# Kernel tuning notes

Measured on AMD Instinct MI355X. Metric: run time of the kernel, lower is better.

## Reference

```python
import jax, jax.numpy as jnp
import numpy as np
from jax import lax

B, T, D, A, H, C, K = 32, 1500, 512, 512, 4, 10, 100  # batch, frames, key/query/value dim, attn dim, heads, conv channels, conv half-kernel


def setup_inputs() -> dict:
    rng = jax.random.key(0)
    ks = jax.random.split(rng, 13)
    s = 0.02  # param init scale
    return {
        "key": jax.random.normal(ks[0], (B, T, D), jnp.float32),
        "key_lens": jax.random.randint(ks[1], (B,), 3 * T // 4, T + 1, jnp.int32),
        "value": jax.random.normal(ks[2], (B, T, D), jnp.float32),
        "query": jax.random.normal(ks[3], (B, 1, D), jnp.float32),
        "aw": jax.random.uniform(ks[4], (H, B, T), jnp.float32),
        # shared-across-heads linear params (ModuleList([m]*n_heads) shares one module)
        "w_enc_W": jax.random.normal(ks[5], (D, A), jnp.float32) * s,
        "w_enc_b": jnp.zeros((A,), jnp.float32),
        "w_dec_W": jax.random.normal(ks[6], (D, A), jnp.float32) * s,
        "w_conv_W": jax.random.normal(ks[7], (C, A), jnp.float32) * s,
        "v_W": jax.random.normal(ks[8], (A,), jnp.float32) * s,
        # distinct conv kernel per head: grouped-conv layout [H*C, 1, 2K+1]
        "conv_W": jax.random.normal(ks[9], (H * C, 1, 2 * K + 1), jnp.float32) * s,
        "w_out_W": jax.random.normal(ks[10], (D * H, D), jnp.float32) * s,
        "w_out_b": jnp.zeros((D,), jnp.float32),
    }


def reference(key, key_lens, value, query, aw, w_enc_W, w_enc_b, w_dec_W,
              w_conv_W, v_W, conv_W, w_out_W, w_out_b):
    bs, key_len, _ = key.shape
    n_heads = aw.shape[0]
    half_k = (conv_W.shape[-1] - 1) // 2

    # key projection (shared weights => identical key_a for every head): [B,T,A]
    key_a = jnp.einsum('btd,da->bta', key, w_enc_W) + w_enc_b
    # query projection (no bias): [B,1,A]
    dec = jnp.einsum('bqd,da->bqa', query, w_dec_W)

    # location conv feature: distinct kernel per head via grouped 1D conv
    x = jnp.transpose(aw, (1, 0, 2))  # [B,H,T]
    conv_out = lax.conv_general_dilated(
        x, conv_W, window_strides=(1,), padding=[(half_k, half_k)],
        feature_group_count=n_heads,
        dimension_numbers=('NCH', 'OIH', 'NCH'))  # [B,H*C,T]
    conv_feat = jnp.transpose(
        conv_out.reshape(bs, n_heads, -1, key_len), (1, 0, 3, 2))  # [H,B,T,C]
    conv_proj = jnp.einsum('hbtc,ca->hbta', conv_feat, w_conv_W)  # [H,B,T,A]

    # additive score with tanh, reduced by v: [H,B,T]
    e = jnp.einsum('hbta,a->hbt',
                   jnp.tanh(key_a[None] + dec[None] + conv_proj), v_W)

    # length mask + softmax (sharpening_factor=1, no sigmoid smoothing)
    mask = jnp.arange(key_len) < key_lens[:, None]  # [B,T]
    e = jnp.where(mask[None], e, -jnp.inf)
    aw_new = jax.nn.softmax(e, axis=-1)  # [H,B,T]

    # NOTE: source uses the INPUT aw for the context (quirk preserved)
    ctx = jnp.einsum('hbt,btv->bhv', aw, value)  # [B,H,V]
    ctx = ctx.reshape(bs, 1, -1)  # head-major concat, [B,1,H*V]
    out = jnp.einsum('bqk,kd->bqd', ctx, w_out_W) + w_out_b  # [B,1,D]
    return out, aw_new
```

## Files before the change

### kernel.cpp

```cpp
#include <hip/hip_runtime.h>
#include <hip/hip_bf16.h>

#define BB 32
#define TT 1500
#define DD 512
#define AA 512
#define HH 4
#define CC 10
#define KK 100
#define KW 201
#define MM (BB*TT)
#define PS 2.8853900817779268f

typedef unsigned short u16;
typedef unsigned int u32;
typedef __attribute__((ext_vector_type(8))) short bf16x8;
typedef __attribute__((ext_vector_type(4))) float f32x4;
typedef __attribute__((ext_vector_type(4))) unsigned int u32x4;

static __device__ __forceinline__ u16 f2bf(float f) {
    u32 x = __float_as_uint(f);
    return (u16)((x + 0x7fffu + ((x >> 16) & 1u)) >> 16);
}
static __device__ __forceinline__ u32 pkbf(float lo, float hi) {
    u32 r;
    asm("v_cvt_pk_bf16_f32 %0, %1, %2" : "=v"(r) : "v"(lo), "v"(hi));
    return r;
}
static __device__ __forceinline__ void stage16(const void* g, void* l) {
    __builtin_amdgcn_global_load_lds(
        (const __attribute__((address_space(1))) void*)g,
        (__attribute__((address_space(3))) void*)l, 16, 0, 0);
}

__global__ __launch_bounds__(256) void prep_k(
    const float* __restrict__ wencW, const float* __restrict__ q,
    const float* __restrict__ wdec, const float* __restrict__ encb,
    const float* __restrict__ aw, const float* __restrict__ convW,
    u16* __restrict__ wenc_t, float* __restrict__ dec_ps,
    float* __restrict__ cfeat, float* __restrict__ ctx, float* __restrict__ outz)
{
    __shared__ float pls[4160];
    int blk = blockIdx.x, tid = threadIdx.x;
    if (blk < 64) {
        int a0 = (blk & 7) * 64, d0 = (blk >> 3) * 64;
#pragma unroll
        for (int it = 0; it < 16; ++it) {
            int row = it * 4 + (tid >> 6), col = tid & 63;
            pls[row * 65 + col] = wencW[(size_t)(d0 + row) * AA + a0 + col];
        }
        __syncthreads();
#pragma unroll
        for (int it = 0; it < 16; ++it) {
            int ar = it * 4 + (tid >> 6), dc = tid & 63;
            wenc_t[(size_t)(a0 + ar) * DD + d0 + dc] = f2bf(pls[dc * 65 + ar] * PS);
        }
    } else if (blk < 128) {
        int bidx = blk - 64;
        int b = bidx >> 1, a = (bidx & 1) * 256 + tid;
        for (int i = tid; i < DD; i += 256) pls[i] = q[b * DD + i];
        __syncthreads();
        float acc = encb[a];
#pragma unroll 8
        for (int d = 0; d < DD; ++d) acc = fmaf(pls[d], wdec[(size_t)d * AA + a], acc);
        dec_ps[b * AA + a] = acc * PS;
    } else if (blk < 384) {
        int cidx = blk - 128;
        int half = cidx & 1, hb = cidx >> 1;
        int h = hb >> 5, b = hb & 31;
        float* srow = pls;
        float* swk  = pls + 952;
        int tstart = half * 750;
        const float* arow = aw + (size_t)(h * BB + b) * TT;
        for (int i = tid; i < 952; i += 256) {
            int t = tstart + i - KK;
            srow[i] = (t >= 0 && t < TT) ? arow[t] : 0.f;
        }
        for (int i = tid; i < CC * KW; i += 256) swk[i] = convW[h * CC * KW + i];
        __syncthreads();
        if (tid < 250) {
            int tl = tid * 3;
            float acc[CC][3];
#pragma unroll
            for (int c = 0; c < CC; ++c)
#pragma unroll
                for (int u = 0; u < 3; ++u) acc[c][u] = 0.f;
            float r0 = srow[tl], r1 = srow[tl + 1], r2 = srow[tl + 2];
            for (int j = 0; j < KW; ++j) {
#pragma unroll
                for (int c = 0; c < CC; ++c) {
                    float w = swk[c * KW + j];
                    acc[c][0] = fmaf(r0, w, acc[c][0]);
                    acc[c][1] = fmaf(r1, w, acc[c][1]);
                    acc[c][2] = fmaf(r2, w, acc[c][2]);
                }
                r0 = r1; r1 = r2; r2 = srow[tl + j + 3];
            }
            float* dst = cfeat + ((size_t)h * MM + (size_t)b * TT + tstart + tl) * CC;
#pragma unroll
            for (int u = 0; u < 3; ++u)
#pragma unroll
                for (int c = 0; c < CC; ++c) dst[u * CC + c] = acc[c][u];
        }
    } else if (blk < 392) {
        float4* p = (float4*)ctx;
        int bidx = blk - 384;
        float4 z = {0.f, 0.f, 0.f, 0.f};
#pragma unroll
        for (int k2 = 0; k2 < 8; ++k2) p[bidx * 2048 + k2 * 256 + tid] = z;
    } else {
        float4* p = (float4*)outz;
        int bidx = blk - 392;
        float4 z = {0.f, 0.f, 0.f, 0.f};
#pragma unroll
        for (int k2 = 0; k2 < 8; ++k2) p[bidx * 2048 + k2 * 256 + tid] = z;
    }
}

__global__ __launch_bounds__(256) void gemm_e_k(
    const float* __restrict__ key, const u16* __restrict__ Bt,
    const float* __restrict__ dec_ps, const float* __restrict__ cf,
    const float* __restrict__ wconv, const float* __restrict__ vw,
    float* __restrict__ Q4)
{
    __shared__ u32x4 smem4[2305];
    char* smem = (char*)smem4;

    int tid = threadIdx.x;
    int orig = blockIdx.x;
    int xcd = orig & 7, idx = orig >> 3;
    int swz = (xcd < 4 ? xcd * 188 : 752 + (xcd - 4) * 187) + idx;
    int bn = swz & 3, bm = swz >> 2;
    int row0 = bm * 128, col0 = bn * 128;
    int lane = tid & 63;
    int wv = tid >> 6;
    int wr = wv >> 1, wc = wv & 1;
    int lhi = lane >> 4, llo = lane & 15;

    f32x4 acc[4][4];
#pragma unroll
    for (int i = 0; i < 4; ++i)
#pragma unroll
        for (int j = 0; j < 4; ++j) acc[i][j] = (f32x4){0.f, 0.f, 0.f, 0.f};

    const float4* gA = (const float4*)(key + (size_t)(row0 + (tid >> 1)) * DD) + (tid & 1) * 4;
    u32 aWoff = (tid >> 1) * 80 + (tid & 1) * 32;
    const u16* gBa = Bt + (size_t)(col0 + (tid & 127)) * DD + (tid >> 7) * 8;
    const u16* gBb = gBa + 16;

    auto loadPA = [&](float4& a0, float4& a1, float4& a2, float4& a3, int s) {
        a0 = gA[s * 8]; a1 = gA[s * 8 + 1]; a2 = gA[s * 8 + 2]; a3 = gA[s * 8 + 3];
    };
    auto stageB = [&](int s, int bbyte) {
        stage16(gBa + s * 32, (u16*)(smem + bbyte) + (size_t)tid * 8);
        stage16(gBb + s * 32, (u16*)(smem + bbyte + 4096) + (size_t)tid * 8);
    };
    auto writeA = [&](int abyte, float4 q0, float4 q1, float4 q2, float4 q3) {
        u32x4 s0, s1;
        s0.x = pkbf(q0.x, q0.y); s0.y = pkbf(q0.z, q0.w);
        s0.z = pkbf(q1.x, q1.y); s0.w = pkbf(q1.z, q1.w);
        s1.x = pkbf(q2.x, q2.y); s1.y = pkbf(q2.z, q2.w);
        s1.z = pkbf(q3.x, q3.y); s1.w = pkbf(q3.z, q3.w);
        *(u32x4*)(smem + abyte + aWoff) = s0;
        *(u32x4*)(smem + abyte + aWoff + 16) = s1;
    };
    auto kstep = [&](int aoff, int boff) {
        bf16x8 af[4], bfr[4];
#pragma unroll
        for (int i = 0; i < 4; ++i)
            af[i] = *(const bf16x8*)(smem + aoff + (wr * 64 + i * 16 + llo) * 80 + lhi * 16);
#pragma unroll
        for (int j = 0; j < 4; ++j)
            bfr[j] = *(const bf16x8*)(smem + boff + (wc * 64 + j * 16 + llo) * 16 + lhi * 2048);
#pragma unroll
        for (int i = 0; i < 4; ++i)
#pragma unroll
            for (int j = 0; j < 4; ++j)
                acc[i][j] = __builtin_amdgcn_mfma_f32_16x16x32_bf16(
                    af[i], bfr[j], acc[i][j], 0, 0, 0);
    };

    float4 e0, e1, e2, e3, o0, o1, o2, o3;
    loadPA(e0, e1, e2, e3, 0);
    stageB(0, 10240);
    writeA(0, e0, e1, e2, e3);
    loadPA(o0, o1, o2, o3, 1);
    loadPA(e0, e1, e2, e3, 2);
    __syncthreads();

#pragma unroll
    for (int t = 0; t < 16; t += 2) {
        stageB(t + 1, 28672);
        writeA(18432, o0, o1, o2, o3);
        if (t + 3 < 16) loadPA(o0, o1, o2, o3, t + 3);
        kstep(0, 10240);
        __syncthreads();
        if (t + 2 < 16) {
            stageB(t + 2, 10240);
            writeA(0, e0, e1, e2, e3);
            if (t + 4 < 16) loadPA(e0, e1, e2, e3, t + 4);
        }
        kstep(18432, 28672);
        __syncthreads();
    }

    const int ZPAD = 36864;
    int b0 = row0 / TT;
    int boundary = (b0 + 1) * TT - row0;
    int b1 = min(b0 + 1, BB - 1);
    {
        int h = tid >> 6;
#pragma unroll
        for (int e = 0; e < 2; ++e) {
            int r = (tid & 63) * 2 + e;
            const float2* cp = (const float2*)(cf + ((size_t)h * MM + row0 + r) * CC);
            float2 c0 = cp[0], c1 = cp[1], c2 = cp[2], c3 = cp[3], c4 = cp[4];
            u32x4 lo, hi;
            lo.x = pkbf(c0.x, c0.y); lo.y = pkbf(c1.x, c1.y);
            lo.z = pkbf(c2.x, c2.y); lo.w = pkbf(c3.x, c3.y);
            hi.x = pkbf(c4.x, c4.y);
            hi.y = (r < boundary) ? 0x00003f80u : 0x3f800000u;
            hi.z = 0u; hi.w = 0u;
            char* dst = smem + (h * 128 + r) * 32;
            *(u32x4*)dst = lo;
            *(u32x4*)(dst + 16) = hi;
        }
        int col = tid >> 1, kh = tid & 1;
        u32x4 w;
        if (kh == 0) {
            float v0 = wconv[0 * AA + col0 + col] * PS, v1 = wconv[1 * AA + col0 + col] * PS;
            float v2 = wconv[2 * AA + col0 + col] * PS, v3 = wconv[3 * AA + col0 + col] * PS;
            float v4 = wconv[4 * AA + col0 + col] * PS, v5 = wconv[5 * AA + col0 + col] * PS;
            float v6 = wconv[6 * AA + col0 + col] * PS, v7 = wconv[7 * AA + col0 + col] * PS;
            w.x = pkbf(v0, v1); w.y = pkbf(v2, v3); w.z = pkbf(v4, v5); w.w = pkbf(v6, v7);
        } else {
            float v8 = wconv[8 * AA + col0 + col] * PS, v9 = wconv[9 * AA + col0 + col] * PS;
            float d0v = dec_ps[b0 * AA + col0 + col], d1v = dec_ps[b1 * AA + col0 + col];
            w.x = pkbf(v8, v9); w.y = pkbf(d0v, d1v); w.z = 0u; w.w = 0u;
        }
        *(u32x4*)(smem + 16384 + col * 32 + kh * 16) = w;
        if (tid == 0) { *(u32x4*)(smem + ZPAD) = (u32x4){0u, 0u, 0u, 0u}; }
    }
    __syncthreads();

    float svj[4];
    bf16x8 be[4];
#pragma unroll
    for (int j = 0; j < 4; ++j) {
        int col = wc * 64 + j * 16 + llo;
        svj[j] = vw[col0 + col];
        u32 off = (lhi < 2) ? (16384u + col * 32 + lhi * 16) : (u32)ZPAD;
        be[j] = *(const bf16x8*)(smem + off);
    }
#pragma unroll
    for (int h = 0; h < 4; ++h) {
#pragma unroll
        for (int i = 0; i < 4; ++i) {
            int rowA = h * 128 + wr * 64 + i * 16 + llo;
            u32 offa = (lhi < 2) ? (rowA * 32 + lhi * 16) : (u32)ZPAD;
            bf16x8 ae = *(const bf16x8*)(smem + offa);
            float ep[4] = {0.f, 0.f, 0.f, 0.f};
#pragma unroll
            for (int j = 0; j < 4; ++j) {
                f32x4 t4 = __builtin_amdgcn_mfma_f32_16x16x32_bf16(ae, be[j], acc[i][j], 0, 0, 0);
#pragma unroll
                for (int r = 0; r < 4; ++r) {
                    float z = exp2f(t4[r]);
                    float p = __builtin_amdgcn_rcpf(1.f + z);
                    ep[r] = fmaf(svj[j], p, ep[r]);
                }
            }
#pragma unroll
            for (int r = 0; r < 4; ++r) {
                float s = ep[r];
                s += __shfl_xor(s, 1);
                s += __shfl_xor(s, 2);
                s += __shfl_xor(s, 4);
                s += __shfl_xor(s, 8);
                if (llo == 0)
                    Q4[((size_t)(bn * HH + h)) * MM + row0 + wr * 64 + i * 16 + lhi * 4 + r] = s;
            }
        }
    }
}

__global__ __launch_bounds__(256) void fin_k(
    const float* __restrict__ Q4, const int* __restrict__ klen,
    const float* __restrict__ aw, const float* __restrict__ value,
    float* __restrict__ aw_new, float* __restrict__ ctx)
{
    __shared__ float fls[1512];
    int blk = blockIdx.x, tid = threadIdx.x;
    if (blk < 128) {
        int h = blk >> 5, b = blk & 31;
        int len = klen[b];
        const float* q0 = Q4 + (size_t)(0 * HH + h) * MM + (size_t)b * TT;
        const float* q1 = Q4 + (size_t)(1 * HH + h) * MM + (size_t)b * TT;
        const float* q2 = Q4 + (size_t)(2 * HH + h) * MM + (size_t)b * TT;
        const float* q3 = Q4 + (size_t)(3 * HH + h) * MM + (size_t)b * TT;
        float* orow = aw_new + (size_t)(h * BB + b) * TT;
        float* rbuf = fls + 1500;
        int lane = tid & 63, wvv = tid >> 6;
        float mx = -3.4e38f;
        for (int t = tid; t < len; t += 256) {
            float e = -2.f * (q0[t] + q1[t] + q2[t] + q3[t]);
            fls[t] = e;
            mx = fmaxf(mx, e);
        }
#pragma unroll
        for (int off = 32; off; off >>= 1) mx = fmaxf(mx, __shfl_xor(mx, off));
        if (lane == 0) rbuf[wvv] = mx;
        __syncthreads();
        mx = fmaxf(fmaxf(rbuf[0], rbuf[1]), fmaxf(rbuf[2], rbuf[3]));
        float sum = 0.f;
        for (int t = tid; t < len; t += 256) {
            float p = __expf(fls[t] - mx);
            fls[t] = p; sum += p;
        }
#pragma unroll
        for (int off = 32; off; off >>= 1) sum += __shfl_xor(sum, off);
        if (lane == 0) rbuf[4 + wvv] = sum;
        __syncthreads();
        float inv = 1.f / (rbuf[4] + rbuf[5] + rbuf[6] + rbuf[7]);
        for (int t = tid; t < TT; t += 256) orow[t] = (t < len) ? fls[t] * inv : 0.f;
    } else {
        int cidx = blk - 128;
        int b = cidx / 25, chunk = cidx - b * 25;
        int c0 = chunk * 60;
        float (*sw)[60] = (float(*)[60])fls;
        if (tid < 240)
            sw[tid / 60][tid % 60] = aw[(size_t)((tid / 60) * BB + b) * TT + c0 + (tid % 60)];
        __syncthreads();
        float a00 = 0, a01 = 0, a10 = 0, a11 = 0, a20 = 0, a21 = 0, a30 = 0, a31 = 0;
        const float* vp = value + ((size_t)b * TT + c0) * DD;
        for (int t = 0; t < 60; ++t) {
            float v0 = vp[(size_t)t * DD + tid];
            float v1 = vp[(size_t)t * DD + tid + 256];
            a00 = fmaf(sw[0][t], v0, a00); a01 = fmaf(sw[0][t], v1, a01);
            a10 = fmaf(sw[1][t], v0, a10); a11 = fmaf(sw[1][t], v1, a11);
            a20 = fmaf(sw[2][t], v0, a20); a21 = fmaf(sw[2][t], v1, a21);
            a30 = fmaf(sw[3][t], v0, a30); a31 = fmaf(sw[3][t], v1, a31);
        }
        atomicAdd(&ctx[(b * HH + 0) * DD + tid], a00);
        atomicAdd(&ctx[(b * HH + 0) * DD + tid + 256], a01);
        atomicAdd(&ctx[(b * HH + 1) * DD + tid], a10);
        atomicAdd(&ctx[(b * HH + 1) * DD + tid + 256], a11);
        atomicAdd(&ctx[(b * HH + 2) * DD + tid], a20);
        atomicAdd(&ctx[(b * HH + 2) * DD + tid + 256], a21);
        atomicAdd(&ctx[(b * HH + 3) * DD + tid], a30);
        atomicAdd(&ctx[(b * HH + 3) * DD + tid + 256], a31);
    }
}

__global__ __launch_bounds__(512) void out_k(const float* __restrict__ ctx,
                                             const float* __restrict__ wout,
                                             const float* __restrict__ wob,
                                             float* __restrict__ out)
{
    int b0 = blockIdx.x * 4, kc = blockIdx.y;
    int tid = threadIdx.x;
    __shared__ float sc[4][64];
    if (tid < 256) sc[tid >> 6][tid & 63] =
        ctx[(size_t)(b0 + (tid >> 6)) * (HH * DD) + kc * 64 + (tid & 63)];
    __syncthreads();
    float acc0 = 0, acc1 = 0, acc2 = 0, acc3 = 0;
    const float* wp = wout + (size_t)(kc * 64) * DD + tid;
#pragma unroll 8
    for (int kk = 0; kk < 64; ++kk) {
        float w = wp[(size_t)kk * DD];
        acc0 = fmaf(sc[0][kk], w, acc0); acc1 = fmaf(sc[1][kk], w, acc1);
        acc2 = fmaf(sc[2][kk], w, acc2); acc3 = fmaf(sc[3][kk], w, acc3);
    }
    if (kc == 0) {
        float bb = wob[tid];
        acc0 += bb; acc1 += bb; acc2 += bb; acc3 += bb;
    }
    atomicAdd(&out[(b0 + 0) * DD + tid], acc0);
    atomicAdd(&out[(b0 + 1) * DD + tid], acc1);
    atomicAdd(&out[(b0 + 2) * DD + tid], acc2);
    atomicAdd(&out[(b0 + 3) * DD + tid], acc3);
}

extern "C" void kernel_launch(void* const* d_in, const int* in_sizes, int n_in,
                              void* d_out, int out_size, void* d_ws, size_t ws_size,
                              hipStream_t stream) {
    const float* key    = (const float*)d_in[0];
    const int*   klen   = (const int*)  d_in[1];
    const float* value  = (const float*)d_in[2];
    const float* query  = (const float*)d_in[3];
    const float* aw     = (const float*)d_in[4];
    const float* wencW  = (const float*)d_in[5];
    const float* wencb  = (const float*)d_in[6];
    const float* wdecW  = (const float*)d_in[7];
    const float* wconvW = (const float*)d_in[8];
    const float* vW     = (const float*)d_in[9];
    const float* convW  = (const float*)d_in[10];
    const float* woutW  = (const float*)d_in[11];
    const float* woutb  = (const float*)d_in[12];

    float* out    = (float*)d_out;
    float* aw_new = out + BB * DD;

    char* ws = (char*)d_ws;
    u16*   wenc_t = (u16*)ws;
    float* dec_ps = (float*)(ws + 524288);
    float* cfeat  = (float*)(ws + 589824);
    float* Q4     = (float*)(ws + 8269824);
    float* ctx    = (float*)(ws + 11341824);

    prep_k  <<<394, 256, 0, stream>>>(wencW, query, wdecW, wencb, aw, convW,
                                      wenc_t, dec_ps, cfeat, ctx, out);
    gemm_e_k<<<1500, 256, 0, stream>>>(key, wenc_t, dec_ps, cfeat, wconvW, vW, Q4);
    fin_k   <<<928, 256, 0, stream>>>(Q4, klen, aw, value, aw_new, ctx);
    out_k   <<<dim3(8, 32), 512, 0, stream>>>(ctx, woutW, woutb, out);
}
```

Baseline: 374.6 us.

## Halve GEMM M-tile to 64 rows and split location conv into more blocks

The fused key-projection/score GEMM now uses 64-row tiles instead of 128, doubling the grid to 3000 blocks. It also shrinks shared memory and moves to a simple double-buffered pipeline with one k-step per iteration. The location-conv stage in the prep kernel is split into 6 chunks per (head,batch) row with one output per thread, increasing block count from 256 to 768. The aim is better occupancy and load balance across the CUs, at the cost of re-reading the B operand more often and less register reuse per thread.

```diff
diff --git a/kernel.cpp b/kernel.cpp
--- a/kernel.cpp
+++ b/kernel.cpp
@@ -64,53 +64,43 @@
 #pragma unroll 8
         for (int d = 0; d < DD; ++d) acc = fmaf(pls[d], wdec[(size_t)d * AA + a], acc);
         dec_ps[b * AA + a] = acc * PS;
-    } else if (blk < 384) {
+    } else if (blk < 896) {
         int cidx = blk - 128;
-        int half = cidx & 1, hb = cidx >> 1;
+        int hb = cidx / 6, chunk = cidx - hb * 6;
         int h = hb >> 5, b = hb & 31;
         float* srow = pls;
-        float* swk  = pls + 952;
-        int tstart = half * 750;
+        float* swk  = pls + 456;
+        int tstart = chunk * 250;
         const float* arow = aw + (size_t)(h * BB + b) * TT;
-        for (int i = tid; i < 952; i += 256) {
+        for (int i = tid; i < 450; i += 256) {
             int t = tstart + i - KK;
             srow[i] = (t >= 0 && t < TT) ? arow[t] : 0.f;
         }
         for (int i = tid; i < CC * KW; i += 256) swk[i] = convW[h * CC * KW + i];
         __syncthreads();
         if (tid < 250) {
-            int tl = tid * 3;
-            float acc[CC][3];
-#pragma unroll
-            for (int c = 0; c < CC; ++c)
-#pragma unroll
-                for (int u = 0; u < 3; ++u) acc[c][u] = 0.f;
-            float r0 = srow[tl], r1 = srow[tl + 1], r2 = srow[tl + 2];
+            float acc[CC];
+#pragma unroll
+            for (int c = 0; c < CC; ++c) acc[c] = 0.f;
             for (int j = 0; j < KW; ++j) {
-#pragma unroll
-                for (int c = 0; c < CC; ++c) {
-                    float w = swk[c * KW + j];
-                    acc[c][0] = fmaf(r0, w, acc[c][0]);
-                    acc[c][1] = fmaf(r1, w, acc[c][1]);
-                    acc[c][2] = fmaf(r2, w, acc[c][2]);
-                }
-                r0 = r1; r1 = r2; r2 = srow[tl + j + 3];
+                float x = srow[tid + j];
+#pragma unroll
+                for (int c = 0; c < CC; ++c)
+                    acc[c] = fmaf(x, swk[c * KW + j], acc[c]);
             }
-            float* dst = cfeat + ((size_t)h * MM + (size_t)b * TT + tstart + tl) * CC;
-#pragma unroll
-            for (int u = 0; u < 3; ++u)
-#pragma unroll
-                for (int c = 0; c < CC; ++c) dst[u * CC + c] = acc[c][u];
-        }
-    } else if (blk < 392) {
+            float* dst = cfeat + ((size_t)h * MM + (size_t)b * TT + tstart + tid) * CC;
+#pragma unroll
+            for (int c = 0; c < CC; ++c) dst[c] = acc[c];
+        }
+    } else if (blk < 904) {
         float4* p = (float4*)ctx;
-        int bidx = blk - 384;
+        int bidx = blk - 896;
         float4 z = {0.f, 0.f, 0.f, 0.f};
 #pragma unroll
         for (int k2 = 0; k2 < 8; ++k2) p[bidx * 2048 + k2 * 256 + tid] = z;
     } else {
         float4* p = (float4*)outz;
-        int bidx = blk - 392;
+        int bidx = blk - 904;
         float4 z = {0.f, 0.f, 0.f, 0.f};
 #pragma unroll
         for (int k2 = 0; k2 < 8; ++k2) p[bidx * 2048 + k2 * 256 + tid] = z;
@@ -123,108 +113,94 @@
     const float* __restrict__ wconv, const float* __restrict__ vw,
     float* __restrict__ Q4)
 {
-    __shared__ u32x4 smem4[2305];
+    __shared__ u32x4 smem4[1665];
     char* smem = (char*)smem4;
 
     int tid = threadIdx.x;
     int orig = blockIdx.x;
     int xcd = orig & 7, idx = orig >> 3;
-    int swz = (xcd < 4 ? xcd * 188 : 752 + (xcd - 4) * 187) + idx;
+    int swz = xcd * 375 + idx;
     int bn = swz & 3, bm = swz >> 2;
-    int row0 = bm * 128, col0 = bn * 128;
-    int lane = tid & 63;
-    int wv = tid >> 6;
+    int row0 = bm * 64, col0 = bn * 128;
+    int lane = tid & 63, wv = tid >> 6;
     int wr = wv >> 1, wc = wv & 1;
     int lhi = lane >> 4, llo = lane & 15;
 
-    f32x4 acc[4][4];
-#pragma unroll
-    for (int i = 0; i < 4; ++i)
+    f32x4 acc[2][4];
+#pragma unroll
+    for (int i = 0; i < 2; ++i)
 #pragma unroll
         for (int j = 0; j < 4; ++j) acc[i][j] = (f32x4){0.f, 0.f, 0.f, 0.f};
 
-    const float4* gA = (const float4*)(key + (size_t)(row0 + (tid >> 1)) * DD) + (tid & 1) * 4;
-    u32 aWoff = (tid >> 1) * 80 + (tid & 1) * 32;
+    const float4* gA = (const float4*)(key + (size_t)(row0 + (tid >> 2)) * DD) + (tid & 3) * 2;
+    u32 aWoff = (tid >> 2) * 80 + (tid & 3) * 16;
     const u16* gBa = Bt + (size_t)(col0 + (tid & 127)) * DD + (tid >> 7) * 8;
     const u16* gBb = gBa + 16;
 
-    auto loadPA = [&](float4& a0, float4& a1, float4& a2, float4& a3, int s) {
-        a0 = gA[s * 8]; a1 = gA[s * 8 + 1]; a2 = gA[s * 8 + 2]; a3 = gA[s * 8 + 3];
-    };
     auto stageB = [&](int s, int bbyte) {
         stage16(gBa + s * 32, (u16*)(smem + bbyte) + (size_t)tid * 8);
         stage16(gBb + s * 32, (u16*)(smem + bbyte + 4096) + (size_t)tid * 8);
     };
-    auto writeA = [&](int abyte, float4 q0, float4 q1, float4 q2, float4 q3) {
-        u32x4 s0, s1;
+    auto writeA = [&](int abyte, float4 q0, float4 q1) {
+        u32x4 s0;
         s0.x = pkbf(q0.x, q0.y); s0.y = pkbf(q0.z, q0.w);
         s0.z = pkbf(q1.x, q1.y); s0.w = pkbf(q1.z, q1.w);
-        s1.x = pkbf(q2.x, q2.y); s1.y = pkbf(q2.z, q2.w);
-        s1.z = pkbf(q3.x, q3.y); s1.w = pkbf(q3.z, q3.w);
         *(u32x4*)(smem + abyte + aWoff) = s0;
-        *(u32x4*)(smem + abyte + aWoff + 16) = s1;
     };
     auto kstep = [&](int aoff, int boff) {
-        bf16x8 af[4], bfr[4];
-#pragma unroll
-        for (int i = 0; i < 4; ++i)
-            af[i] = *(const bf16x8*)(smem + aoff + (wr * 64 + i * 16 + llo) * 80 + lhi * 16);
+        bf16x8 af[2], bfr[4];
+#pragma unroll
+        for (int i = 0; i < 2; ++i)
+            af[i] = *(const bf16x8*)(smem + aoff + (wr * 32 + i * 16 + llo) * 80 + lhi * 16);
 #pragma unroll
         for (int j = 0; j < 4; ++j)
             bfr[j] = *(const bf16x8*)(smem + boff + (wc * 64 + j * 16 + llo) * 16 + lhi * 2048);
 #pragma unroll
-        for (int i = 0; i < 4; ++i)
+        for (int i = 0; i < 2; ++i)
 #pragma unroll
             for (int j = 0; j < 4; ++j)
                 acc[i][j] = __builtin_amdgcn_mfma_f32_16x16x32_bf16(
                     af[i], bfr[j], acc[i][j], 0, 0, 0);
     };
 
-    float4 e0, e1, e2, e3, o0, o1, o2, o3;
-    loadPA(e0, e1, e2, e3, 0);
+    float4 p0 = gA[0], p1 = gA[1];
     stageB(0, 10240);
-    writeA(0, e0, e1, e2, e3);
-    loadPA(o0, o1, o2, o3, 1);
-    loadPA(e0, e1, e2, e3, 2);
+    writeA(0, p0, p1);
+    p0 = gA[8]; p1 = gA[9];
     __syncthreads();
 
 #pragma unroll
-    for (int t = 0; t < 16; t += 2) {
-        stageB(t + 1, 28672);
-        writeA(18432, o0, o1, o2, o3);
-        if (t + 3 < 16) loadPA(o0, o1, o2, o3, t + 3);
-        kstep(0, 10240);
-        __syncthreads();
-        if (t + 2 < 16) {
-            stageB(t + 2, 10240);
-            writeA(0, e0, e1, e2, e3);
-            if (t + 4 < 16) loadPA(e0, e1, e2, e3, t + 4);
-        }
-        kstep(18432, 28672);
-        __syncthreads();
-    }
-
-    const int ZPAD = 36864;
+    for (int t = 0; t < 16; ++t) {
+        const int abuf_c = (t & 1) ? 5120 : 0;
+        const int bbuf_c = (t & 1) ? 18432 : 10240;
+        if (t < 15) {
+            const int abuf_n = (t & 1) ? 0 : 5120;
+            const int bbuf_n = (t & 1) ? 10240 : 18432;
+            stageB(t + 1, bbuf_n);
+            writeA(abuf_n, p0, p1);
+            if (t < 14) { p0 = gA[(t + 2) * 8]; p1 = gA[(t + 2) * 8 + 1]; }
+        }
+        kstep(abuf_c, bbuf_c);
+        __syncthreads();
+    }
+
+    const int ZPAD = 26624;
     int b0 = row0 / TT;
     int boundary = (b0 + 1) * TT - row0;
     int b1 = min(b0 + 1, BB - 1);
     {
-        int h = tid >> 6;
-#pragma unroll
-        for (int e = 0; e < 2; ++e) {
-            int r = (tid & 63) * 2 + e;
-            const float2* cp = (const float2*)(cf + ((size_t)h * MM + row0 + r) * CC);
-            float2 c0 = cp[0], c1 = cp[1], c2 = cp[2], c3 = cp[3], c4 = cp[4];
-            u32x4 lo, hi;
-            lo.x = pkbf(c0.x, c0.y); lo.y = pkbf(c1.x, c1.y);
-            lo.z = pkbf(c2.x, c2.y); lo.w = pkbf(c3.x, c3.y);
-            hi.x = pkbf(c4.x, c4.y);
-            hi.y = (r < boundary) ? 0x00003f80u : 0x3f800000u;
-            hi.z = 0u; hi.w = 0u;
-            char* dst = smem + (h * 128 + r) * 32;
-            *(u32x4*)dst = lo;
-            *(u32x4*)(dst + 16) = hi;
-        }
+        int h = tid >> 6, r = tid & 63;
+        const float2* cp = (const float2*)(cf + ((size_t)h * MM + row0 + r) * CC);
+        float2 c0 = cp[0], c1 = cp[1], c2 = cp[2], c3 = cp[3], c4 = cp[4];
+        u32x4 lo, hi;
+        lo.x = pkbf(c0.x, c0.y); lo.y = pkbf(c1.x, c1.y);
+        lo.z = pkbf(c2.x, c2.y); lo.w = pkbf(c3.x, c3.y);
+        hi.x = pkbf(c4.x, c4.y);
+        hi.y = (r < boundary) ? 0x00003f80u : 0x3f800000u;
+        hi.z = 0u; hi.w = 0u;
+        char* dst = smem + (h * 64 + r) * 48;
+        *(u32x4*)dst = lo;
+        *(u32x4*)(dst + 16) = hi;
         int col = tid >> 1, kh = tid & 1;
         u32x4 w;
         if (kh == 0) {
@@ -238,7 +214,7 @@
             float d0v = dec_ps[b0 * AA + col0 + col], d1v = dec_ps[b1 * AA + col0 + col];
             w.x = pkbf(v8, v9); w.y = pkbf(d0v, d1v); w.z = 0u; w.w = 0u;
         }
-        *(u32x4*)(smem + 16384 + col * 32 + kh * 16) = w;
+        *(u32x4*)(smem + 12288 + col * 48 + kh * 16) = w;
         if (tid == 0) { *(u32x4*)(smem + ZPAD) = (u32x4){0u, 0u, 0u, 0u}; }
     }
     __syncthreads();
@@ -249,15 +225,15 @@
     for (int j = 0; j < 4; ++j) {
         int col = wc * 64 + j * 16 + llo;
         svj[j] = vw[col0 + col];
-        u32 off = (lhi < 2) ? (16384u + col * 32 + lhi * 16) : (u32)ZPAD;
+        u32 off = (lhi < 2) ? (12288u + col * 48 + lhi * 16) : (u32)ZPAD;
         be[j] = *(const bf16x8*)(smem + off);
     }
 #pragma unroll
     for (int h = 0; h < 4; ++h) {
 #pragma unroll
-        for (int i = 0; i < 4; ++i) {
-            int rowA = h * 128 + wr * 64 + i * 16 + llo;
-            u32 offa = (lhi < 2) ? (rowA * 32 + lhi * 16) : (u32)ZPAD;
+        for (int i = 0; i < 2; ++i) {
+            int rowA = h * 64 + wr * 32 + i * 16 + llo;
+            u32 offa = (lhi < 2) ? (rowA * 48 + lhi * 16) : (u32)ZPAD;
             bf16x8 ae = *(const bf16x8*)(smem + offa);
             float ep[4] = {0.f, 0.f, 0.f, 0.f};
 #pragma unroll
@@ -278,7 +254,7 @@
                 s += __shfl_xor(s, 4);
                 s += __shfl_xor(s, 8);
                 if (llo == 0)
-                    Q4[((size_t)(bn * HH + h)) * MM + row0 + wr * 64 + i * 16 + lhi * 4 + r] = s;
+                    Q4[((size_t)(bn * HH + h)) * MM + row0 + wr * 32 + i * 16 + lhi * 4 + r] = s;
             }
         }
     }
@@ -408,9 +384,9 @@
     float* Q4     = (float*)(ws + 8269824);
     float* ctx    = (float*)(ws + 11341824);
 
-    prep_k  <<<394, 256, 0, stream>>>(wencW, query, wdecW, wencb, aw, convW,
+    prep_k  <<<906, 256, 0, stream>>>(wencW, query, wdecW, wencb, aw, convW,
                                       wenc_t, dec_ps, cfeat, ctx, out);
-    gemm_e_k<<<1500, 256, 0, stream>>>(key, wenc_t, dec_ps, cfeat, wconvW, vW, Q4);
+    gemm_e_k<<<3000, 256, 0, stream>>>(key, wenc_t, dec_ps, cfeat, wconvW, vW, Q4);
     fin_k   <<<928, 256, 0, stream>>>(Q4, klen, aw, value, aw_new, ctx);
     out_k   <<<dim3(8, 32), 512, 0, stream>>>(ctx, woutW, woutb, out);
 }
```

After: 360.5 us. 1.04x faster.
